# Performance work log

Hardware: AMD Instinct MI355X
Metric: run time of the kernel (lower is better)

The kernel has to match this reference:

```python
import jax, jax.numpy as jnp
import numpy as np

D = 256; NH = 8; HD = D // NH; NP = 4; NL = 3; R = 8
SHAPES = ((64, 64), (32, 32), (16, 16))
SUMHW = sum(h * w for h, w in SHAPES)  # 5376
LQ = R + SUMHW                          # 5384
B = 2; FH = FW = 128; EPS = 1e-6; HID = 4 * D


def _ln(x, w):
    m = jnp.mean(x, axis=-1, keepdims=True)
    v = jnp.mean((x - m) ** 2, axis=-1, keepdims=True)
    return (x - m) * jax.lax.rsqrt(v + EPS) * w


def _mlp(x, fc1_w, fc2_w, star_s, star_b):
    h = jnp.maximum(x @ fc1_w.T, 0.0)
    h = star_s * h * h + star_b  # StarReLU
    return h @ fc2_w.T


def _interp_bilinear(x, oh, ow):
    # x: (B, H, W, C); torch F.interpolate bilinear align_corners=False
    b, h, w, c = x.shape
    def coords(o, n):
        src = (jnp.arange(o, dtype=jnp.float32) + 0.5) * (n / o) - 0.5
        src = jnp.maximum(src, 0.0)
        i0 = jnp.minimum(jnp.floor(src).astype(jnp.int32), n - 1)
        i1 = jnp.minimum(i0 + 1, n - 1)
        return i0, i1, src - i0
    y0, y1, ty = coords(oh, h)
    x0, x1, tx = coords(ow, w)
    ty = ty[None, :, None, None]; tx = tx[None, None, :, None]
    top = x[:, y0][:, :, x0] * (1 - tx) + x[:, y0][:, :, x1] * tx
    bot = x[:, y1][:, :, x0] * (1 - tx) + x[:, y1][:, :, x1] * tx
    return top * (1 - ty) + bot * ty


def _conv3x3(x, w, b):
    return jax.lax.conv_general_dilated(
        x, w, window_strides=(1, 1), padding='SAME',
        dimension_numbers=('NHWC', 'HWIO', 'NHWC')) + b


def _deform_attn(query, value_src, ref, Wv, bv, Woff, boff, Wattn, battn, Wout, bout):
    # query: (B, LQ, D); value_src: (B, SUMHW, D); ref: (B, LQ, NL, 2) in [0,1]
    b = query.shape[0]
    value = (value_src @ Wv.T + bv).reshape(b, SUMHW, NH, HD)
    off = (query @ Woff.T + boff).reshape(b, LQ, NH, NL, NP, 2)
    aw = jax.nn.softmax((query @ Wattn.T + battn).reshape(b, LQ, NH, NL * NP), axis=-1)
    aw = aw.reshape(b, LQ, NH, NL, NP)
    normalizer = jnp.array([[w_, h_] for (h_, w_) in SHAPES], jnp.float32)  # (NL,2) as (W,H)
    loc = ref[:, :, None, :, None, :] + off / normalizer[None, None, None, :, None, :]
    out = jnp.zeros((b, NH, LQ, HD), query.dtype)
    start = 0
    for l, (H, W) in enumerate(SHAPES):
        v_l = value[:, start:start + H * W].transpose(0, 2, 1, 3)  # (B,NH,HW,HD)
        start += H * W
        loc_l = loc[:, :, :, l]                                     # (B,LQ,NH,NP,2)
        x = loc_l[..., 0] * W - 0.5
        y = loc_l[..., 1] * H - 0.5
        x0 = jnp.floor(x); y0 = jnp.floor(y)
        lx = (x - x0).transpose(0, 2, 1, 3)[..., None]  # (B,NH,LQ,NP,1)
        ly = (y - y0).transpose(0, 2, 1, 3)[..., None]
        x0i = x0.astype(jnp.int32); y0i = y0.astype(jnp.int32)
        def gather(xi, yi):
            valid = (xi >= 0) & (xi < W) & (yi >= 0) & (yi < H)
            idx = jnp.clip(yi, 0, H - 1) * W + jnp.clip(xi, 0, W - 1)
            idx_t = idx.transpose(0, 2, 1, 3).reshape(b, NH, LQ * NP, 1)
            g = jnp.take_along_axis(v_l, idx_t, axis=2).reshape(b, NH, LQ, NP, HD)
            return g * valid.transpose(0, 2, 1, 3)[..., None]
        samp = (gather(x0i, y0i) * (1 - lx) * (1 - ly)
                + gather(x0i + 1, y0i) * lx * (1 - ly)
                + gather(x0i, y0i + 1) * (1 - lx) * ly
                + gather(x0i + 1, y0i + 1) * lx * ly)
        w_l = aw[:, :, :, l].transpose(0, 2, 1, 3)[..., None]  # (B,NH,LQ,NP,1)
        out = out + jnp.sum(samp * w_l, axis=3)
    out = out.transpose(0, 2, 1, 3).reshape(b, LQ, D)
    return out @ Wout.T + bout


def setup_inputs() -> dict:
    key = jax.random.key(0)
    ks = jax.random.split(key, 20)
    s = 0.02
    return {
        'src': jax.random.normal(ks[0], (B, LQ, D), jnp.float32),
        'pos': jax.random.normal(ks[1], (B, LQ, D), jnp.float32),
        'fpn': jax.random.normal(ks[2], (B, FH, FW, D), jnp.float32),
        'reference_points': jax.random.uniform(ks[3], (B, LQ, NL, 2), jnp.float32),
        'spatial_shapes': jnp.array(SHAPES, jnp.int32),
        'norm1_w': jnp.ones((D,), jnp.float32),
        'norm2_w': jnp.ones((D,), jnp.float32),
        'Wv': jax.random.normal(ks[4], (D, D), jnp.float32) * s,
        'bv': jnp.zeros((D,), jnp.float32),
        'Woff': jax.random.normal(ks[5], (NH * NL * NP * 2, D), jnp.float32) * s,
        'boff': jax.random.normal(ks[6], (NH * NL * NP * 2,), jnp.float32) * 0.5,
        'Wattn': jax.random.normal(ks[7], (NH * NL * NP, D), jnp.float32) * s,
        'battn': jnp.zeros((NH * NL * NP,), jnp.float32),
        'Wout': jax.random.normal(ks[8], (D, D), jnp.float32) * s,
        'bout': jnp.zeros((D,), jnp.float32),
        'conv_w': jax.random.normal(ks[9], (3, 3, 3, D, D), jnp.float32) * s,
        'conv_b': jnp.zeros((3, D), jnp.float32),
        'fc1_w': jax.random.normal(ks[10], (HID, D), jnp.float32) * s,
        'fc2_w': jax.random.normal(ks[11], (D, HID), jnp.float32) * s,
        'star_s': jnp.float32(1.0),
        'star_b': jnp.float32(0.0),
    }


def reference(src, pos, fpn, reference_points, spatial_shapes, norm1_w, norm2_w,
              Wv, bv, Woff, boff, Wattn, battn, Wout, bout, conv_w, conv_b,
              fc1_w, fc2_w, star_s, star_b):
    hw_lens = [h * w for h, w in SHAPES]
    src2 = _ln(src, norm1_w)
    fpn2 = _ln(fpn, norm1_w)
    # deformable cross attention: queries = registers + spatial tokens; value = spatial tokens
    src2 = _deform_attn(src2 + pos, src2[:, R:], reference_points,
                        Wv, bv, Woff, boff, Wattn, battn, Wout, bout)
    # split spatial part into per-scale BHWC maps
    hw = src2[:, R:]
    feats, start = [], 0
    for (h, w) in SHAPES:
        feats.append(hw[:, start:start + h * w].reshape(-1, h, w, D))
        start += h * w
    # top-down FPN fusion: coarse (res5) -> fine (res2)
    ret = [fpn2] + feats       # [res2, res3, res4, res5]
    ret = ret[::-1]            # [res5, res4, res3, res2]
    out = ret[0]
    for i, f in enumerate(ret[1:]):
        f = f + _interp_bilinear(out, f.shape[1], f.shape[2])
        out = _conv3x3(f, conv_w[i], conv_b[i])
    fpn_fused = out            # fused res2 (B,FH,FW,D)
    # residuals + MLP (drop_path = 0 -> identity)
    src_out = src + src2
    fpn_out = fpn + fpn_fused
    src_out = src_out + _mlp(_ln(src_out, norm2_w), fc1_w, fc2_w, star_s, star_b)
    fpn_out = fpn_out + _mlp(_ln(fpn_out, norm2_w), fc1_w, fc2_w, star_s, star_b)
    return (src_out, fpn_out)
```

## Files before the change

### kernel.cpp

```cpp
#include <hip/hip_runtime.h>
#include <hip/hip_bf16.h>

#define D_      256
#define NH_     8
#define HD_     32
#define NP_     4
#define NL_     3
#define RTOK    8
#define LQ_     5384
#define SUMHW_  5376
#define B_      2
#define FH_     128
#define HID_    1024
#define EPS_    1e-6f

#define OFF_S2  0
#define OFF_QB  2756608
#define OFF_VB  5513216
#define OFF_OB  8265728
#define OFF_AW  10333184
#define OFF_CA  5513216
#define OFF_CB  13901824
#define OFF_W1B 22290432
#define OFF_W2B 22421504
#define OFF_CWB 22552576
#define OFF_WVB 23437312
#define OFF_WOFB 23470080
#define OFF_WATB 23494656
#define OFF_WOUB 23511040

typedef __attribute__((ext_vector_type(4))) float f32x4;
typedef __attribute__((ext_vector_type(8))) short short8;
typedef __attribute__((ext_vector_type(4))) unsigned short ushort4_;

__device__ __forceinline__ unsigned short f2bf(float f) {
    unsigned u = __float_as_uint(f);
    unsigned r = u + 0x7fff + ((u >> 16) & 1);
    return (unsigned short)(r >> 16);
}

__device__ __forceinline__ float blk_sum(float v, float* scr) {
    #pragma unroll
    for (int o = 32; o > 0; o >>= 1) v += __shfl_down(v, o, 64);
    int w = threadIdx.x >> 6;
    if ((threadIdx.x & 63) == 0) scr[w] = v;
    __syncthreads();
    float s = scr[0] + scr[1] + scr[2] + scr[3];
    __syncthreads();
    return s;
}

__global__ __launch_bounds__(256)
void k_cvt_pad(const float* __restrict__ src, unsigned short* __restrict__ dst,
               int nreal, int ntot) {
    int i = blockIdx.x * 256 + threadIdx.x;
    if (i < ntot) dst[i] = (i < nreal) ? f2bf(src[i]) : (unsigned short)0;
}

__global__ __launch_bounds__(256)
void k_conv_w_prep(const float* __restrict__ convw, unsigned short* __restrict__ dst) {
    int i = blockIdx.x * 256 + threadIdx.x;
    int ci = i & 255;
    int co = (i >> 8) & 255;
    int kk = i >> 16;
    dst[(size_t)kk * 65536 + co * 256 + ci] = f2bf(convw[(size_t)kk * 65536 + ci * 256 + co]);
}

__global__ __launch_bounds__(256)
void k_ln_src(const float* __restrict__ src, const float* __restrict__ pos,
              const float* __restrict__ w1, float* __restrict__ S2, float* __restrict__ QB) {
    size_t row = blockIdx.x;
    int c = threadIdx.x;
    __shared__ float scr[4];
    float v = src[row * D_ + c];
    float mean = blk_sum(v, scr) * (1.0f / D_);
    float d = v - mean;
    float var = blk_sum(d * d, scr) * (1.0f / D_);
    float y = d * rsqrtf(var + EPS_) * w1[c];
    S2[row * D_ + c] = y;
    QB[row * D_ + c] = y + pos[row * D_ + c];
}

template<int NCHUNK>
__global__ __launch_bounds__(256)
void k_gemm_mfma(const float* __restrict__ A, long long a_bstride,
                 const unsigned short* __restrict__ Wb,
                 const float* __restrict__ bias, float* __restrict__ C,
                 long long c_bstride, int M, int N) {
    __shared__ unsigned short buf[16384];
    int b = blockIdx.y;
    const float* Ab = A + (size_t)b * a_bstride;
    float* Cb = C + (size_t)b * c_bstride;
    int r0 = blockIdx.x * 64;
    int tid = threadIdx.x;
    int w = tid >> 6, l = tid & 63;

    for (int g = tid; g < 2048; g += 256) {
        int r = g >> 5, e8 = g & 31;
        int row = r0 + r;
        float4 v0 = make_float4(0.f,0.f,0.f,0.f), v1 = v0;
        if (row < M) {
            v0 = *(const float4*)&Ab[(size_t)row * 256 + e8 * 8];
            v1 = *(const float4*)&Ab[(size_t)row * 256 + e8 * 8 + 4];
        }
        short8 p;
        p[0]=f2bf(v0.x); p[1]=f2bf(v0.y); p[2]=f2bf(v0.z); p[3]=f2bf(v0.w);
        p[4]=f2bf(v1.x); p[5]=f2bf(v1.y); p[6]=f2bf(v1.z); p[7]=f2bf(v1.w);
        *(short8*)&buf[r * 256 + ((e8 * 8) ^ ((r & 7) << 3))] = p;
    }
    __syncthreads();
    int rA = 16 * w + (l & 15);
    int kA = (l >> 4) * 8;
    int swzA = (rA & 7) << 3;
    short8 af[8];
    #pragma unroll
    for (int ks = 0; ks < 8; ++ks)
        af[ks] = *(const short8*)&buf[rA * 256 + ((kA + ks * 32) ^ swzA)];
    __syncthreads();

    for (int nc = 0; nc < NCHUNK; ++nc) {
        for (int g = tid; g < 2048; g += 256) {
            int n = g >> 5, e8 = g & 31;
            short8 p = *(const short8*)&Wb[(size_t)(nc * 64 + n) * 256 + e8 * 8];
            *(short8*)&buf[n * 256 + ((e8 * 8) ^ ((n & 7) << 3))] = p;
        }
        __syncthreads();
        f32x4 acc[4];
        #pragma unroll
        for (int i = 0; i < 4; ++i) acc[i] = (f32x4){0.f,0.f,0.f,0.f};
        #pragma unroll
        for (int ks = 0; ks < 8; ++ks) {
            #pragma unroll
            for (int ct = 0; ct < 4; ++ct) {
                int n = ct * 16 + (l & 15);
                short8 bf = *(const short8*)&buf[n * 256 + ((kA + ks * 32) ^ ((n & 7) << 3))];
                acc[ct] = __builtin_amdgcn_mfma_f32_16x16x32_bf16(af[ks], bf, acc[ct], 0, 0, 0);
            }
        }
        #pragma unroll
        for (int ct = 0; ct < 4; ++ct) {
            int n = nc * 64 + ct * 16 + (l & 15);
            if (n < N) {
                float bb = bias ? bias[n] : 0.f;
                #pragma unroll
                for (int q = 0; q < 4; ++q) {
                    int row = r0 + 16 * w + (l >> 4) * 4 + q;
                    if (row < M) Cb[(size_t)row * N + n] = acc[ct][q] + bb;
                }
            }
        }
        __syncthreads();
    }
}

__global__ __launch_bounds__(256)
void k_softmax12(float* __restrict__ AW, int total) {
    int t = blockIdx.x * 256 + threadIdx.x;
    if (t >= total) return;
    float* p = AW + (size_t)t * 12;
    float m = p[0];
    #pragma unroll
    for (int i = 1; i < 12; ++i) m = fmaxf(m, p[i]);
    float s = 0.f;
    float e[12];
    #pragma unroll
    for (int i = 0; i < 12; ++i) { e[i] = __expf(p[i] - m); s += e[i]; }
    float inv = 1.f / s;
    #pragma unroll
    for (int i = 0; i < 12; ++i) p[i] = e[i] * inv;
}

__global__ __launch_bounds__(256)
void k_sample(const float* __restrict__ VB, const float* __restrict__ OB,
              const float* __restrict__ AW, const float* __restrict__ refp,
              float* __restrict__ AT) {
    int bq = blockIdx.x;
    int b  = bq / LQ_;
    int h  = threadIdx.x >> 5;
    int dd = threadIdx.x & 31;
    const float* off = OB + (size_t)bq * 192;
    const float* aw  = AW + (size_t)bq * 96;
    const float* rp  = refp + (size_t)bq * (NL_ * 2);
    const int HS[3] = {64, 32, 16};
    const int ST[3] = {0, 4096, 5120};
    float acc = 0.f;
    #pragma unroll
    for (int l = 0; l < NL_; ++l) {
        float rx = rp[l * 2 + 0], ry = rp[l * 2 + 1];
        int Wl = HS[l], Hl = HS[l];
        float fWl = (float)Wl, fHl = (float)Hl;
        const float* vbase = VB + ((size_t)b * SUMHW_ + ST[l]) * D_ + h * 32 + dd;
        #pragma unroll
        for (int p = 0; p < NP_; ++p) {
            int oi = ((h * NL_ + l) * NP_ + p) * 2;
            float locx = rx + off[oi]     / fWl;
            float locy = ry + off[oi + 1] / fHl;
            float x = locx * fWl - 0.5f;
            float y = locy * fHl - 0.5f;
            float x0f = floorf(x), y0f = floorf(y);
            float fx = x - x0f, fy = y - y0f;
            int x0 = (int)x0f, y0 = (int)y0f;
            float a = aw[(h * NL_ + l) * NP_ + p];
            float g = 0.f;
            if (x0 >= 0     && x0 < Wl     && y0 >= 0     && y0 < Hl)
                g += (1.f - fx) * (1.f - fy) * vbase[(size_t)(y0 * Wl + x0) * D_];
            if (x0 + 1 >= 0 && x0 + 1 < Wl && y0 >= 0     && y0 < Hl)
                g += fx * (1.f - fy) * vbase[(size_t)(y0 * Wl + x0 + 1) * D_];
            if (x0 >= 0     && x0 < Wl     && y0 + 1 >= 0 && y0 + 1 < Hl)
                g += (1.f - fx) * fy * vbase[(size_t)((y0 + 1) * Wl + x0) * D_];
            if (x0 + 1 >= 0 && x0 + 1 < Wl && y0 + 1 >= 0 && y0 + 1 < Hl)
                g += fx * fy * vbase[(size_t)((y0 + 1) * Wl + x0 + 1) * D_];
            acc += a * g;
        }
    }
    AT[(size_t)bq * D_ + threadIdx.x] = acc;
}

__global__ __launch_bounds__(256)
void k_build_f(const float* __restrict__ feat, long long feat_bstride, int do_ln,
               const float* __restrict__ w1,
               const float* __restrict__ prev, long long prev_bstride, int PH, int PW,
               float* __restrict__ out, int OH, int OW) {
    int idx = blockIdx.x;
    int x = idx % OW;
    int y = (idx / OW) % OH;
    int b = idx / (OW * OH);
    int c = threadIdx.x;
    __shared__ float scr[4];
    float fv = feat[(size_t)b * feat_bstride + (size_t)(y * OW + x) * D_ + c];
    if (do_ln) {
        float mean = blk_sum(fv, scr) * (1.0f / D_);
        float d = fv - mean;
        float var = blk_sum(d * d, scr) * (1.0f / D_);
        fv = d * rsqrtf(var + EPS_) * w1[c];
    }
    float sy = fmaxf((y + 0.5f) * ((float)PH / OH) - 0.5f, 0.f);
    int y0 = min((int)floorf(sy), PH - 1);
    int y1 = min(y0 + 1, PH - 1);
    float ty = sy - (float)y0;
    float sx = fmaxf((x + 0.5f) * ((float)PW / OW) - 0.5f, 0.f);
    int x0 = min((int)floorf(sx), PW - 1);
    int x1 = min(x0 + 1, PW - 1);
    float tx = sx - (float)x0;
    const float* pb = prev + (size_t)b * prev_bstride;
    float v00 = pb[(size_t)(y0 * PW + x0) * D_ + c];
    float v01 = pb[(size_t)(y0 * PW + x1) * D_ + c];
    float v10 = pb[(size_t)(y1 * PW + x0) * D_ + c];
    float v11 = pb[(size_t)(y1 * PW + x1) * D_ + c];
    float top = v00 * (1.f - tx) + v01 * tx;
    float bot = v10 * (1.f - tx) + v11 * tx;
    out[(size_t)idx * D_ + c] = fv + (top * (1.f - ty) + bot * ty);
}

template<int SW>
__global__ __launch_bounds__(256)
void k_conv_mfma(const float* __restrict__ in, const unsigned short* __restrict__ wb,
                 const float* __restrict__ bias, float* __restrict__ out, int H, int W) {
    constexpr int CX = SW + 2;
    constexpr int NCT = (SW == 64) ? 4 : 2;
    __shared__ unsigned short tile[CX * 256];
    __shared__ unsigned short wbuf[64 * 256];
    int nxb = W / SW;
    int bid = blockIdx.x;
    int x0 = (bid % nxb) * SW;
    int y  = (bid / nxb) % H;
    int b  = bid / (nxb * H);
    int tid = threadIdx.x, w = tid >> 6, l = tid & 63;
    const float* ib = in + (size_t)b * H * W * 256;

    int RT    = (SW == 64) ? w : (w & 1);
    int ctoff = (SW == 64) ? 0 : ((w >> 1) * 2);
    int kA = (l >> 4) * 8;

    f32x4 acc[4 * NCT];
    #pragma unroll
    for (int i = 0; i < 4 * NCT; ++i) acc[i] = (f32x4){0.f, 0.f, 0.f, 0.f};

    for (int ky = 0; ky < 3; ++ky) {
        int gy = y + ky - 1;
        __syncthreads();
        for (int t = tid; t < CX * 32; t += 256) {
            int cx = t >> 5;
            int e8 = (t & 31) * 8;
            int gx = x0 + cx - 1;
            float4 v0 = make_float4(0.f,0.f,0.f,0.f), v1 = v0;
            if (gy >= 0 && gy < H && gx >= 0 && gx < W) {
                v0 = *(const float4*)&ib[((size_t)gy * W + gx) * 256 + e8];
                v1 = *(const float4*)&ib[((size_t)gy * W + gx) * 256 + e8 + 4];
            }
            short8 p;
            p[0]=f2bf(v0.x); p[1]=f2bf(v0.y); p[2]=f2bf(v0.z); p[3]=f2bf(v0.w);
            p[4]=f2bf(v1.x); p[5]=f2bf(v1.y); p[6]=f2bf(v1.z); p[7]=f2bf(v1.w);
            *(short8*)&tile[cx * 256 + (e8 ^ ((cx & 7) << 3))] = p;
        }
        __syncthreads();
        for (int kx = 0; kx < 3; ++kx) {
            short8 af[8];
            int cx = RT * 16 + (l & 15) + kx;
            int swz = (cx & 7) << 3;
            #pragma unroll
            for (int ks = 0; ks < 8; ++ks)
                af[ks] = *(const short8*)&tile[cx * 256 + ((ks * 32 + kA) ^ swz)];
            const unsigned short* wt = wb + (size_t)(ky * 3 + kx) * 65536;
            for (int nc = 0; nc < 4; ++nc) {
                __syncthreads();
                for (int g = tid; g < 2048; g += 256) {
                    int n = g >> 5, e8 = (g & 31) * 8;
                    short8 p = *(const short8*)&wt[(size_t)(nc * 64 + n) * 256 + e8];
                    *(short8*)&wbuf[n * 256 + (e8 ^ ((n & 7) << 3))] = p;
                }
                __syncthreads();
                #pragma unroll
                for (int ks = 0; ks < 8; ++ks) {
                    #pragma unroll
                    for (int j = 0; j < NCT; ++j) {
                        int n = (ctoff + j) * 16 + (l & 15);
                        short8 bf = *(const short8*)&wbuf[n * 256 + ((ks * 32 + kA) ^ ((n & 7) << 3))];
                        acc[nc * NCT + j] = __builtin_amdgcn_mfma_f32_16x16x32_bf16(af[ks], bf, acc[nc * NCT + j], 0, 0, 0);
                    }
                }
            }
        }
    }
    size_t orow = ((size_t)b * H + y) * W;
    #pragma unroll
    for (int q = 0; q < 4; ++q) {
        int px = x0 + RT * 16 + (l >> 4) * 4 + q;
        #pragma unroll
        for (int nc = 0; nc < 4; ++nc) {
            #pragma unroll
            for (int j = 0; j < NCT; ++j) {
                int n = nc * 64 + (ctoff + j) * 16 + (l & 15);
                out[(orow + px) * 256 + n] = acc[nc * NCT + j][q] + bias[n];
            }
        }
    }
}

__global__ __launch_bounds__(256)
void k_mlp_mfma(const float* __restrict__ a, const float* __restrict__ bsrc,
                const float* __restrict__ n2,
                const unsigned short* __restrict__ W1b, const unsigned short* __restrict__ W2b,
                const float* __restrict__ ssp, const float* __restrict__ sbp,
                float* __restrict__ out, int M) {
    __shared__ unsigned short buf[32768];
    __shared__ unsigned short Hc[4096];
    int r0 = blockIdx.x * 64;
    int tid = threadIdx.x;
    int w = tid >> 6;
    int l = tid & 63;
    float ss = ssp[0], sb = sbp[0];

    #pragma unroll 4
    for (int i = 0; i < 16; ++i) {
        int r = w * 16 + i;
        int row = r0 + r;
        float4 xa = make_float4(0.f,0.f,0.f,0.f), xb = xa;
        if (row < M) {
            xa = *(const float4*)&a[(size_t)row * 256 + l * 4];
            xb = *(const float4*)&bsrc[(size_t)row * 256 + l * 4];
        }
        float v0 = xa.x + xb.x, v1 = xa.y + xb.y, v2 = xa.z + xb.z, v3 = xa.w + xb.w;
        float s = v0 + v1 + v2 + v3;
        #pragma unroll
        for (int o = 32; o > 0; o >>= 1) s += __shfl_xor(s, o);
        float mean = s * (1.f / 256.f);
        float d0 = v0 - mean, d1 = v1 - mean, d2 = v2 - mean, d3 = v3 - mean;
        float vv = d0 * d0 + d1 * d1 + d2 * d2 + d3 * d3;
        #pragma unroll
        for (int o = 32; o > 0; o >>= 1) vv += __shfl_xor(vv, o);
        float rs = rsqrtf(vv * (1.f / 256.f) + EPS_);
        float4 nw = *(const float4*)&n2[l * 4];
        ushort4_ p;
        p.x = f2bf(d0 * rs * nw.x); p.y = f2bf(d1 * rs * nw.y);
        p.z = f2bf(d2 * rs * nw.z); p.w = f2bf(d3 * rs * nw.w);
        *(ushort4_*)&buf[r * 256 + ((l * 4) ^ ((r & 7) << 3))] = p;
    }
    __syncthreads();
    int rA = 16 * w + (l & 15);
    int kA = (l >> 4) * 8;
    int swzA = (rA & 7) << 3;
    short8 af[8];
    #pragma unroll
    for (int ks = 0; ks < 8; ++ks)
        af[ks] = *(const short8*)&buf[rA * 256 + ((kA + ks * 32) ^ swzA)];
    __syncthreads();

    f32x4 oacc[16];
    #pragma unroll
    for (int i = 0; i < 16; ++i) oacc[i] = (f32x4){0.f,0.f,0.f,0.f};

    for (int nc = 0; nc < 16; ++nc) {
        for (int g = tid; g < 2048; g += 256) {
            int n = g >> 5, e8 = g & 31;
            short8 p = *(const short8*)&W1b[(size_t)(nc * 64 + n) * 256 + e8 * 8];
            *(short8*)&buf[n * 256 + ((e8 * 8) ^ ((n & 7) << 3))] = p;
        }
        for (int g = tid; g < 2048; g += 256) {
            int o = g >> 3, kb = g & 7;
            short8 p = *(const short8*)&W2b[(size_t)o * 1024 + nc * 64 + kb * 8];
            *(short8*)&buf[16384 + o * 64 + ((kb * 8) ^ ((o & 7) << 3))] = p;
        }
        __syncthreads();
        f32x4 hacc[4];
        #pragma unroll
        for (int i = 0; i < 4; ++i) hacc[i] = (f32x4){0.f,0.f,0.f,0.f};
        #pragma unroll
        for (int ks = 0; ks < 8; ++ks) {
            #pragma unroll
            for (int ct = 0; ct < 4; ++ct) {
                int n = ct * 16 + (l & 15);
                short8 bf = *(const short8*)&buf[n * 256 + ((kA + ks * 32) ^ ((n & 7) << 3))];
                hacc[ct] = __builtin_amdgcn_mfma_f32_16x16x32_bf16(af[ks], bf, hacc[ct], 0, 0, 0);
            }
        }
        #pragma unroll
        for (int ct = 0; ct < 4; ++ct) {
            #pragma unroll
            for (int q = 0; q < 4; ++q) {
                float hv = fmaxf(hacc[ct][q], 0.f);
                hv = ss * hv * hv + sb;
                int rr = (l >> 4) * 4 + q;
                int cc = ct * 16 + (l & 15);
                Hc[w * 1024 + rr * 64 + (cc ^ ((rr & 7) << 3))] = f2bf(hv);
            }
        }
        #pragma unroll
        for (int ks2 = 0; ks2 < 2; ++ks2) {
            short8 af2 = *(const short8*)&Hc[w * 1024 + (l & 15) * 64 + ((kA + ks2 * 32) ^ (((l & 15) & 7) << 3))];
            #pragma unroll
            for (int ot = 0; ot < 16; ++ot) {
                int o = ot * 16 + (l & 15);
                short8 bf2 = *(const short8*)&buf[16384 + o * 64 + ((kA + ks2 * 32) ^ ((o & 7) << 3))];
                oacc[ot] = __builtin_amdgcn_mfma_f32_16x16x32_bf16(af2, bf2, oacc[ot], 0, 0, 0);
            }
        }
        __syncthreads();
    }
    #pragma unroll
    for (int q = 0; q < 4; ++q) {
        int row = r0 + 16 * w + (l >> 4) * 4 + q;
        if (row < M) {
            #pragma unroll
            for (int ot = 0; ot < 16; ++ot) {
                int col = ot * 16 + (l & 15);
                size_t off = (size_t)row * 256 + col;
                out[off] = a[off] + bsrc[off] + oacc[ot][q];
            }
        }
    }
}

extern "C" void kernel_launch(void* const* d_in, const int* in_sizes, int n_in,
                              void* d_out, int out_size, void* d_ws, size_t ws_size,
                              hipStream_t stream) {
    const float* src   = (const float*)d_in[0];
    const float* pos   = (const float*)d_in[1];
    const float* fpn   = (const float*)d_in[2];
    const float* refp  = (const float*)d_in[3];
    const float* n1w   = (const float*)d_in[5];
    const float* n2w   = (const float*)d_in[6];
    const float* Wv    = (const float*)d_in[7];
    const float* bv    = (const float*)d_in[8];
    const float* Woff  = (const float*)d_in[9];
    const float* boff  = (const float*)d_in[10];
    const float* Wattn = (const float*)d_in[11];
    const float* battn = (const float*)d_in[12];
    const float* Wout  = (const float*)d_in[13];
    const float* bout  = (const float*)d_in[14];
    const float* convw = (const float*)d_in[15];
    const float* convb = (const float*)d_in[16];
    const float* fc1   = (const float*)d_in[17];
    const float* fc2   = (const float*)d_in[18];
    const float* ssp   = (const float*)d_in[19];
    const float* sbp   = (const float*)d_in[20];

    float* ws = (float*)d_ws;
    float* S2 = ws + OFF_S2;
    float* QB = ws + OFF_QB;
    float* VB = ws + OFF_VB;
    float* OB = ws + OFF_OB;
    float* AW = ws + OFF_AW;
    float* CA = ws + OFF_CA;
    float* CB = ws + OFF_CB;
    unsigned short* W1B = (unsigned short*)(ws + OFF_W1B);
    unsigned short* W2B = (unsigned short*)(ws + OFF_W2B);
    unsigned short* CWB = (unsigned short*)(ws + OFF_CWB);
    unsigned short* WVB = (unsigned short*)(ws + OFF_WVB);
    unsigned short* WOFB = (unsigned short*)(ws + OFF_WOFB);
    unsigned short* WATB = (unsigned short*)(ws + OFF_WATB);
    unsigned short* WOUB = (unsigned short*)(ws + OFF_WOUB);
    float* out = (float*)d_out;

    k_cvt_pad<<<1024, 256, 0, stream>>>(fc1, W1B, 262144, 262144);
    k_cvt_pad<<<1024, 256, 0, stream>>>(fc2, W2B, 262144, 262144);
    k_conv_w_prep<<<(1769472 + 255) / 256, 256, 0, stream>>>(convw, CWB);
    k_cvt_pad<<<256, 256, 0, stream>>>(Wv, WVB, 65536, 65536);
    k_cvt_pad<<<192, 256, 0, stream>>>(Woff, WOFB, 49152, 49152);
    k_cvt_pad<<<128, 256, 0, stream>>>(Wattn, WATB, 24576, 32768);
    k_cvt_pad<<<256, 256, 0, stream>>>(Wout, WOUB, 65536, 65536);

    k_ln_src<<<B_ * LQ_, 256, 0, stream>>>(src, pos, n1w, S2, QB);

    k_gemm_mfma<4><<<dim3(SUMHW_ / 64, B_), 256, 0, stream>>>(
        S2 + (size_t)RTOK * D_, (long long)LQ_ * D_, WVB, bv,
        VB, (long long)SUMHW_ * D_, SUMHW_, 256);

    k_gemm_mfma<3><<<dim3((B_ * LQ_ + 63) / 64, 1), 256, 0, stream>>>(
        QB, 0, WOFB, boff, OB, 0, B_ * LQ_, 192);
    k_gemm_mfma<2><<<dim3((B_ * LQ_ + 63) / 64, 1), 256, 0, stream>>>(
        QB, 0, WATB, battn, AW, 0, B_ * LQ_, 96);
    k_softmax12<<<(B_ * LQ_ * NH_ + 255) / 256, 256, 0, stream>>>(AW, B_ * LQ_ * NH_);

    k_sample<<<B_ * LQ_, 256, 0, stream>>>(VB, OB, AW, refp, QB);

    k_gemm_mfma<4><<<dim3((B_ * LQ_ + 63) / 64, 1), 256, 0, stream>>>(
        QB, 0, WOUB, bout, S2, 0, B_ * LQ_, 256);

    k_build_f<<<B_ * 32 * 32, 256, 0, stream>>>(
        S2 + (size_t)(RTOK + 4096) * D_, (long long)LQ_ * D_, 0, n1w,
        S2 + (size_t)(RTOK + 5120) * D_, (long long)LQ_ * D_, 16, 16,
        CA, 32, 32);
    k_conv_mfma<32><<<32 * B_, 256, 0, stream>>>(CA, CWB, convb, CB, 32, 32);
    k_build_f<<<B_ * 64 * 64, 256, 0, stream>>>(
        S2 + (size_t)RTOK * D_, (long long)LQ_ * D_, 0, n1w,
        CB, (long long)32 * 32 * D_, 32, 32,
        CA, 64, 64);
    k_conv_mfma<64><<<64 * B_, 256, 0, stream>>>(CA, CWB + (size_t)9 * 65536, convb + D_, CB, 64, 64);
    k_build_f<<<B_ * 128 * 128, 256, 0, stream>>>(
        fpn, (long long)FH_ * FH_ * D_, 1, n1w,
        CB, (long long)64 * 64 * D_, 64, 64,
        CA, 128, 128);
    k_conv_mfma<64><<<2 * 128 * B_, 256, 0, stream>>>(CA, CWB + (size_t)18 * 65536, convb + 2 * D_, CB, 128, 128);

    k_mlp_mfma<<<(B_ * LQ_ + 63) / 64, 256, 0, stream>>>(src, S2, n2w, W1B, W2B, ssp, sbp,
                                                         out, B_ * LQ_);
    k_mlp_mfma<<<(B_ * FH_ * FH_) / 64, 256, 0, stream>>>(fpn, CB, n2w, W1B, W2B, ssp, sbp,
                                                          out + (size_t)B_ * LQ_ * D_, B_ * FH_ * FH_);
}
```

Measured before the change: 959.5 us.

## Register-prefetch weight chunks and widen LDS swizzle in MFMA GEMM, conv, MLP

Loads the next 64x256 bf16 weight chunk into registers while the current chunk is being consumed, in the GEMM, conv3x3 and MLP kernels, so global-load latency overlaps MFMA work instead of stalling behind a barrier. It also widens the XOR swizzle from 8 to 16 rows and pads the W2 LDS rows to 72 elements to reduce bank conflicts. The cost is 8 extra short8 registers per thread, which may lower occupancy, plus a slightly larger LDS footprint in the MLP. The prefetch assumes contiguous weight chunk layout, so the conv code walks all 36 chunks in order.

```diff
diff --git a/kernel.cpp b/kernel.cpp
--- a/kernel.cpp
+++ b/kernel.cpp
@@ -95,6 +95,13 @@
     int tid = threadIdx.x;
     int w = tid >> 6, l = tid & 63;
 
+    short8 R[8];
+    {
+        const short8* p = (const short8*)Wb;
+        #pragma unroll
+        for (int i = 0; i < 8; ++i) R[i] = p[tid + i * 256];
+    }
+
     for (int g = tid; g < 2048; g += 256) {
         int r = g >> 5, e8 = g & 31;
         int row = r0 + r;
@@ -106,12 +113,12 @@
         short8 p;
         p[0]=f2bf(v0.x); p[1]=f2bf(v0.y); p[2]=f2bf(v0.z); p[3]=f2bf(v0.w);
         p[4]=f2bf(v1.x); p[5]=f2bf(v1.y); p[6]=f2bf(v1.z); p[7]=f2bf(v1.w);
-        *(short8*)&buf[r * 256 + ((e8 * 8) ^ ((r & 7) << 3))] = p;
+        *(short8*)&buf[r * 256 + ((e8 * 8) ^ ((r & 15) << 3))] = p;
     }
     __syncthreads();
     int rA = 16 * w + (l & 15);
     int kA = (l >> 4) * 8;
-    int swzA = (rA & 7) << 3;
+    int swzA = (rA & 15) << 3;
     short8 af[8];
     #pragma unroll
     for (int ks = 0; ks < 8; ++ks)
@@ -119,10 +126,16 @@
     __syncthreads();
 
     for (int nc = 0; nc < NCHUNK; ++nc) {
-        for (int g = tid; g < 2048; g += 256) {
-            int n = g >> 5, e8 = g & 31;
-            short8 p = *(const short8*)&Wb[(size_t)(nc * 64 + n) * 256 + e8 * 8];
-            *(short8*)&buf[n * 256 + ((e8 * 8) ^ ((n & 7) << 3))] = p;
+        #pragma unroll
+        for (int i = 0; i < 8; ++i) {
+            int g = tid + i * 256;
+            int n = g >> 5, e8 = (g & 31) * 8;
+            *(short8*)&buf[n * 256 + (e8 ^ ((n & 15) << 3))] = R[i];
+        }
+        if (nc + 1 < NCHUNK) {
+            const short8* p = (const short8*)(Wb + (size_t)(nc + 1) * 16384);
+            #pragma unroll
+            for (int i = 0; i < 8; ++i) R[i] = p[tid + i * 256];
         }
         __syncthreads();
         f32x4 acc[4];
@@ -133,7 +146,7 @@
             #pragma unroll
             for (int ct = 0; ct < 4; ++ct) {
                 int n = ct * 16 + (l & 15);
-                short8 bf = *(const short8*)&buf[n * 256 + ((kA + ks * 32) ^ ((n & 7) << 3))];
+                short8 bf = *(const short8*)&buf[n * 256 + ((kA + ks * 32) ^ ((n & 15) << 3))];
                 acc[ct] = __builtin_amdgcn_mfma_f32_16x16x32_bf16(af[ks], bf, acc[ct], 0, 0, 0);
             }
         }
@@ -276,6 +289,14 @@
     #pragma unroll
     for (int i = 0; i < 4 * NCT; ++i) acc[i] = (f32x4){0.f, 0.f, 0.f, 0.f};
 
+    short8 R[8];
+    {
+        const short8* p = (const short8*)wb;
+        #pragma unroll
+        for (int i = 0; i < 8; ++i) R[i] = p[tid + i * 256];
+    }
+    int c = 0;
+
     for (int ky = 0; ky < 3; ++ky) {
         int gy = y + ky - 1;
         __syncthreads();
@@ -291,23 +312,28 @@
             short8 p;
             p[0]=f2bf(v0.x); p[1]=f2bf(v0.y); p[2]=f2bf(v0.z); p[3]=f2bf(v0.w);
             p[4]=f2bf(v1.x); p[5]=f2bf(v1.y); p[6]=f2bf(v1.z); p[7]=f2bf(v1.w);
-            *(short8*)&tile[cx * 256 + (e8 ^ ((cx & 7) << 3))] = p;
+            *(short8*)&tile[cx * 256 + (e8 ^ ((cx & 15) << 3))] = p;
         }
         __syncthreads();
         for (int kx = 0; kx < 3; ++kx) {
             short8 af[8];
             int cx = RT * 16 + (l & 15) + kx;
-            int swz = (cx & 7) << 3;
+            int swz = (cx & 15) << 3;
             #pragma unroll
             for (int ks = 0; ks < 8; ++ks)
                 af[ks] = *(const short8*)&tile[cx * 256 + ((ks * 32 + kA) ^ swz)];
-            const unsigned short* wt = wb + (size_t)(ky * 3 + kx) * 65536;
             for (int nc = 0; nc < 4; ++nc) {
-                __syncthreads();
-                for (int g = tid; g < 2048; g += 256) {
+                #pragma unroll
+                for (int i = 0; i < 8; ++i) {
+                    int g = tid + i * 256;
                     int n = g >> 5, e8 = (g & 31) * 8;
-                    short8 p = *(const short8*)&wt[(size_t)(nc * 64 + n) * 256 + e8];
-                    *(short8*)&wbuf[n * 256 + (e8 ^ ((n & 7) << 3))] = p;
+                    *(short8*)&wbuf[n * 256 + (e8 ^ ((n & 15) << 3))] = R[i];
+                }
+                ++c;
+                if (c < 36) {
+                    const short8* p = (const short8*)(wb + (size_t)c * 16384);
+                    #pragma unroll
+                    for (int i = 0; i < 8; ++i) R[i] = p[tid + i * 256];
                 }
                 __syncthreads();
                 #pragma unroll
@@ -315,10 +341,11 @@
                     #pragma unroll
                     for (int j = 0; j < NCT; ++j) {
                         int n = (ctoff + j) * 16 + (l & 15);
-                        short8 bf = *(const short8*)&wbuf[n * 256 + ((ks * 32 + kA) ^ ((n & 7) << 3))];
+                        short8 bf = *(const short8*)&wbuf[n * 256 + ((ks * 32 + kA) ^ ((n & 15) << 3))];
                         acc[nc * NCT + j] = __builtin_amdgcn_mfma_f32_16x16x32_bf16(af[ks], bf, acc[nc * NCT + j], 0, 0, 0);
                     }
                 }
+                __syncthreads();
             }
         }
     }
@@ -343,13 +370,20 @@
                 const unsigned short* __restrict__ W1b, const unsigned short* __restrict__ W2b,
                 const float* __restrict__ ssp, const float* __restrict__ sbp,
                 float* __restrict__ out, int M) {
-    __shared__ unsigned short buf[32768];
+    __shared__ unsigned short buf[34816];
     __shared__ unsigned short Hc[4096];
     int r0 = blockIdx.x * 64;
     int tid = threadIdx.x;
     int w = tid >> 6;
     int l = tid & 63;
     float ss = ssp[0], sb = sbp[0];
+
+    short8 R1[8];
+    {
+        const short8* p = (const short8*)W1b;
+        #pragma unroll
+        for (int i = 0; i < 8; ++i) R1[i] = p[tid + i * 256];
+    }
 
     #pragma unroll 4
     for (int i = 0; i < 16; ++i) {
@@ -374,12 +408,12 @@
         ushort4_ p;
         p.x = f2bf(d0 * rs * nw.x); p.y = f2bf(d1 * rs * nw.y);
         p.z = f2bf(d2 * rs * nw.z); p.w = f2bf(d3 * rs * nw.w);
-        *(ushort4_*)&buf[r * 256 + ((l * 4) ^ ((r & 7) << 3))] = p;
+        *(ushort4_*)&buf[r * 256 + ((l * 4) ^ ((r & 15) << 3))] = p;
     }
     __syncthreads();
     int rA = 16 * w + (l & 15);
     int kA = (l >> 4) * 8;
-    int swzA = (rA & 7) << 3;
+    int swzA = (rA & 15) << 3;
     short8 af[8];
     #pragma unroll
     for (int ks = 0; ks < 8; ++ks)
@@ -391,15 +425,21 @@
     for (int i = 0; i < 16; ++i) oacc[i] = (f32x4){0.f,0.f,0.f,0.f};
 
     for (int nc = 0; nc < 16; ++nc) {
-        for (int g = tid; g < 2048; g += 256) {
-            int n = g >> 5, e8 = g & 31;
-            short8 p = *(const short8*)&W1b[(size_t)(nc * 64 + n) * 256 + e8 * 8];
-            *(short8*)&buf[n * 256 + ((e8 * 8) ^ ((n & 7) << 3))] = p;
+        #pragma unroll
+        for (int i = 0; i < 8; ++i) {
+            int g = tid + i * 256;
+            int n = g >> 5, e8 = (g & 31) * 8;
+            *(short8*)&buf[n * 256 + (e8 ^ ((n & 15) << 3))] = R1[i];
+        }
+        if (nc + 1 < 16) {
+            const short8* p = (const short8*)(W1b + (size_t)(nc + 1) * 16384);
+            #pragma unroll
+            for (int i = 0; i < 8; ++i) R1[i] = p[tid + i * 256];
         }
         for (int g = tid; g < 2048; g += 256) {
             int o = g >> 3, kb = g & 7;
             short8 p = *(const short8*)&W2b[(size_t)o * 1024 + nc * 64 + kb * 8];
-            *(short8*)&buf[16384 + o * 64 + ((kb * 8) ^ ((o & 7) << 3))] = p;
+            *(short8*)&buf[16384 + o * 72 + ((kb * 8) ^ ((o & 7) << 3))] = p;
         }
         __syncthreads();
         f32x4 hacc[4];
@@ -410,7 +450,7 @@
             #pragma unroll
             for (int ct = 0; ct < 4; ++ct) {
                 int n = ct * 16 + (l & 15);
-                short8 bf = *(const short8*)&buf[n * 256 + ((kA + ks * 32) ^ ((n & 7) << 3))];
+                short8 bf = *(const short8*)&buf[n * 256 + ((kA + ks * 32) ^ ((n & 15) << 3))];
                 hacc[ct] = __builtin_amdgcn_mfma_f32_16x16x32_bf16(af[ks], bf, hacc[ct], 0, 0, 0);
             }
         }
@@ -431,7 +471,7 @@
             #pragma unroll
             for (int ot = 0; ot < 16; ++ot) {
                 int o = ot * 16 + (l & 15);
-                short8 bf2 = *(const short8*)&buf[16384 + o * 64 + ((kA + ks2 * 32) ^ ((o & 7) << 3))];
+                short8 bf2 = *(const short8*)&buf[16384 + o * 72 + ((kA + ks2 * 32) ^ ((o & 7) << 3))];
                 oacc[ot] = __builtin_amdgcn_mfma_f32_16x16x32_bf16(af2, bf2, oacc[ot], 0, 0, 0);
             }
         }
```

New measurement: 823.7 us. 14.2% less time.
